# Kernel optimization log

Measured on AMD Instinct MI355X. Metric: run time of the kernel, lower is better.

## Reference

```python
import jax, jax.numpy as jnp
import numpy as np

D = 1024        # embedding_dim
N = 200000      # number of train embeddings
C = 50          # n_concepts
B = 4096        # batch size
NUM_CLASSES = 4
TOPK = 50


def setup_inputs() -> dict:
    key = jax.random.key(0)
    k1, k2, k3, k4, k5 = jax.random.split(key, 5)
    return {
        "concept": jax.random.normal(k1, (D, C), dtype=jnp.float32),
        "train_embeddings": jax.random.normal(k2, (D, N), dtype=jnp.float32),
        "train_embedding": jax.random.normal(k3, (B, D), dtype=jnp.float32),
        "hx_weight": jax.random.normal(k4, (NUM_CLASSES, D), dtype=jnp.float32) * 0.02,
        "hx_bias": jax.random.normal(k5, (NUM_CLASSES,), dtype=jnp.float32) * 0.02,
        "topk": TOPK,
    }


def reference(concept, train_embeddings, train_embedding, hx_weight, hx_bias, topk):
    n_concepts = concept.shape[1]
    k = int(topk)

    # projection of inputs onto concept subspace: P = C (C^T C)^{-1} C^T
    gram = concept.T @ concept                      # (C, C)
    proj_matrix = concept @ jnp.linalg.inv(gram) @ concept.T   # (D, D)
    proj = proj_matrix @ train_embedding.T          # (D, B)
    y_pred = proj.T @ hx_weight.T + hx_bias         # (B, num_classes)
    orig_pred = train_embedding @ hx_weight.T + hx_bias

    # batched KNN: squared euclidean distance of every concept to every train embedding
    # (sqrt is monotone, ordering identical to torch.norm-based distances)
    te_sq = jnp.sum(train_embeddings * train_embeddings, axis=0)   # (N,)
    c_sq = jnp.sum(concept * concept, axis=0)                      # (C,)
    dots = concept.T @ train_embeddings                            # (C, N)
    dist2 = c_sq[:, None] + te_sq[None, :] - 2.0 * dots            # (C, N)
    _, knn_idx = jax.lax.top_k(-dist2, k)                          # (C, k) smallest distances

    # gather neighbor activations: (D, C, k)
    knn_act = jnp.take(train_embeddings, knn_idx.reshape(-1), axis=1).reshape(
        train_embeddings.shape[0], n_concepts, k)

    # L_sparse_1 = mean_c [ sum_{d,k} concept[d,c]*knn[d,c,k] / k ]
    L_sparse_1 = jnp.einsum("dc,dck->", concept, knn_act) / (k * n_concepts)

    eye = jnp.eye(n_concepts, dtype=concept.dtype)
    mask = 1.0 - eye
    L_sparse_2 = jnp.mean(gram * mask)
    norm_metrics = jnp.mean(gram * eye)
    similarity_penalty = jnp.mean(jnp.abs(gram - eye))

    return (orig_pred, y_pred, L_sparse_1, L_sparse_2, norm_metrics, similarity_penalty)
```

## Files before the change

### kernel.cpp

```cpp
#include <hip/hip_runtime.h>
#include <stdint.h>

#define D 1024
#define N 200000
#define C 50
#define B 4096
#define CLS 4
#define KParts 16
#define CAP 4096
#define BN 512
#define NBLK 391
#define NSLOT (NBLK * 8)

typedef __attribute__((ext_vector_type(8))) short short8;
typedef __attribute__((ext_vector_type(4))) float f32x4;

static const size_t OFF_U     = 0;
static const size_t OFF_TESQ  = (size_t)C * N;
static const size_t OFF_GPART = OFF_TESQ + N;
static const size_t OFF_WPART = OFF_GPART + KParts * 2500;
static const size_t OFF_ABF   = ((OFF_WPART + KParts * 200 + 3) / 4) * 4;
static const size_t OFF_RANGE = OFF_ABF + 32768;
static const size_t OFF_SUMS  = OFF_RANGE + 2 * NSLOT;
static const size_t OFF_CNT   = OFF_SUMS + C;
static const size_t OFF_W8    = ((OFF_CNT + 1 + 3) / 4) * 4;

__device__ __forceinline__ unsigned mapf(float v) {
    unsigned u = __float_as_uint(v);
    return (u & 0x80000000u) ? ~u : (u | 0x80000000u);
}
__device__ __forceinline__ float unmapf(unsigned u) {
    unsigned b = (u & 0x80000000u) ? (u ^ 0x80000000u) : ~u;
    return __uint_as_float(b);
}
__device__ __forceinline__ unsigned keyu(float dot, float tesq) {
    return mapf(fmaf(-2.0f, dot, tesq));
}
__device__ __forceinline__ unsigned short f2bf(float f) {
    unsigned u = __float_as_uint(f);
    u += 0x7FFFu + ((u >> 16) & 1u);
    return (unsigned short)(u >> 16);
}
__device__ __forceinline__ float bf2f(unsigned short h) {
    return __uint_as_float((unsigned)h << 16);
}

__global__ __launch_bounds__(256) void kprep(
    const float* __restrict__ concept, const float* __restrict__ hxw,
    float* __restrict__ ws)
{
    int t = threadIdx.x;

    if (blockIdx.x < KParts) {
        __shared__ __align__(16) float ct[64 * 50];
        __shared__ float hs[4 * 64];
        int bid = blockIdx.x;
        int d0 = bid * 64;

        for (int i = t; i < 64 * 50; i += 256) ct[i] = concept[d0 * 50 + i];
        {
            int j = t >> 6, dd = t & 63;
            hs[t] = hxw[j * D + d0 + dd];
        }
        __syncthreads();

        float* gp = ws + OFF_GPART + (size_t)bid * 2500;
        for (int p = t; p < 2500; p += 256) {
            int i = p / 50, j = p - i * 50;
            float acc = 0.f;
            #pragma unroll 8
            for (int dd = 0; dd < 64; ++dd)
                acc = fmaf(ct[dd * 50 + i], ct[dd * 50 + j], acc);
            gp[p] = acc;
        }
        float* wp = ws + OFF_WPART + (size_t)bid * 200;
        if (t < 200) {
            int j = t / 50, c = t - j * 50;
            float acc = 0.f;
            #pragma unroll 8
            for (int dd = 0; dd < 64; ++dd)
                acc = fmaf(hs[j * 64 + dd], ct[dd * 50 + c], acc);
            wp[t] = acc;
        }
        return;
    }

    unsigned short* ap = (unsigned short*)(ws + OFF_ABF);
    for (int idx = t; idx < 8192; idx += 256) {
        int ks = idx >> 8;
        int g  = (idx >> 6) & 3;
        int m  = idx & 63;
        unsigned short v[8];
        #pragma unroll
        for (int j = 0; j < 8; ++j) {
            int k = ks * 32 + g * 8 + j;
            v[j] = (m < 50) ? f2bf(concept[k * 50 + m]) : (unsigned short)0;
        }
        uint4 pk;
        pk.x = (unsigned)v[0] | ((unsigned)v[1] << 16);
        pk.y = (unsigned)v[2] | ((unsigned)v[3] << 16);
        pk.z = (unsigned)v[4] | ((unsigned)v[5] << 16);
        pk.w = (unsigned)v[6] | ((unsigned)v[7] << 16);
        *(uint4*)(ap + (size_t)idx * 8) = pk;
    }
}

__global__ __launch_bounds__(512) void kgemm(
    const float* __restrict__ concept, const float* __restrict__ te,
    const float* __restrict__ hxw, float* __restrict__ ws,
    float* __restrict__ out)
{
    __shared__ unsigned Bl[16 * 516];
    __shared__ __align__(16) unsigned short Al[4 * 64 * 8];
    __shared__ float tsp[4][BN];
    __shared__ float tsf[BN];
    __shared__ float gsh[2500];
    __shared__ float Asv[50 * 56];
    __shared__ float colp[C];
    __shared__ float part[3][8];

    int t = threadIdx.x;
    int l = t & 63, w = t >> 6;

    if (blockIdx.x == NBLK) {
        if (t == 0) ((unsigned*)(ws + OFF_CNT))[0] = 0u;

        float s_all = 0.f, s_tr = 0.f, s_abs = 0.f;
        for (int p = t; p < 2500; p += 512) {
            float g = 0.f;
            #pragma unroll
            for (int b = 0; b < KParts; ++b)
                g += ws[OFF_GPART + (size_t)b * 2500 + p];
            gsh[p] = g;
            int i = p / 50, jj = p - i * 50;
            float e = (i == jj) ? 1.0f : 0.0f;
            s_all += g;
            if (i == jj) s_tr += g;
            s_abs += fabsf(g - e);
        }
        #pragma unroll
        for (int off = 32; off > 0; off >>= 1) {
            s_all += __shfl_down(s_all, off, 64);
            s_tr  += __shfl_down(s_tr,  off, 64);
            s_abs += __shfl_down(s_abs, off, 64);
        }
        if (l == 0) { part[0][w] = s_all; part[1][w] = s_tr; part[2][w] = s_abs; }
        __syncthreads();
        if (t == 0) {
            float a = 0.f, tr = 0.f, ab = 0.f;
            for (int i = 0; i < 8; ++i) { a += part[0][i]; tr += part[1][i]; ab += part[2][i]; }
            out[32769] = (a - tr) / 2500.0f;
            out[32770] = tr / 2500.0f;
            out[32771] = ab / 2500.0f;
        }

        for (int p = t; p < 50 * 56; p += 512) {
            int r = p / 56, col = p - r * 56;
            float v = 0.f;
            if (col < 50) v = gsh[r * 50 + col];
            else if (col < 54) {
                float ww = 0.f;
                #pragma unroll
                for (int b = 0; b < KParts; ++b)
                    ww += ws[OFF_WPART + (size_t)b * 200 + (col - 50) * 50 + r];
                v = ww;
            }
            Asv[p] = v;
        }
        __syncthreads();

        for (int pc = 0; pc < C; ++pc) {
            if (t < C) colp[t] = Asv[t * 56 + pc];
            __syncthreads();
            float pinv = 1.0f / colp[pc];
            if (t < 56) Asv[pc * 56 + t] *= pinv;
            __syncthreads();
            for (int p = t; p < 50 * 56; p += 512) {
                int r = p / 56, col = p - r * 56;
                if (r != pc) Asv[p] = fmaf(-colp[r], Asv[pc * 56 + col], Asv[p]);
            }
            __syncthreads();
        }

        for (int d = t; d < D; d += 512) {
            float wy0 = 0.f, wy1 = 0.f, wy2 = 0.f, wy3 = 0.f;
            for (int c = 0; c < C; ++c) {
                float cv = concept[d * 50 + c];
                wy0 = fmaf(cv, Asv[c * 56 + 50], wy0);
                wy1 = fmaf(cv, Asv[c * 56 + 51], wy1);
                wy2 = fmaf(cv, Asv[c * 56 + 52], wy2);
                wy3 = fmaf(cv, Asv[c * 56 + 53], wy3);
            }
            float4 lo, hi;
            lo.x = hxw[0 * D + d]; lo.y = hxw[1 * D + d];
            lo.z = hxw[2 * D + d]; lo.w = hxw[3 * D + d];
            hi.x = wy0; hi.y = wy1; hi.z = wy2; hi.w = wy3;
            *(float4*)(ws + OFF_W8 + (size_t)d * 8)     = lo;
            *(float4*)(ws + OFF_W8 + (size_t)d * 8 + 4) = hi;
        }
        return;
    }

    int nbase = blockIdx.x * BN;
    int nq = t & 127, rp = t >> 7;
    int ncol0 = nbase + nq * 4;
    bool colv = (ncol0 < N);

    f32x4 accf[4][4];
    #pragma unroll
    for (int mf = 0; mf < 4; ++mf)
        #pragma unroll
        for (int nf = 0; nf < 4; ++nf)
            accf[mf][nf] = (f32x4)(0.0f);
    float ts0 = 0.f, ts1 = 0.f, ts2 = 0.f, ts3 = 0.f;

    const unsigned short* ap = (const unsigned short*)(ws + OFF_ABF);
    int g = l >> 4;

    #pragma unroll 1
    for (int ks = 0; ks < 32; ++ks) {
        __syncthreads();
        if (t < 256) {
            uint4 av = *(const uint4*)(ap + ((size_t)ks * 256 + t) * 8);
            *(uint4*)(Al + t * 8) = av;
        }
        #pragma unroll
        for (int pi = 0; pi < 4; ++pi) {
            int pair = rp + pi * 4;
            int k0 = ks * 32 + pair * 2;
            float4 xa, xb;
            if (colv) {
                xa = *(const float4*)(te + (size_t)k0 * N + ncol0);
                xb = *(const float4*)(te + (size_t)(k0 + 1) * N + ncol0);
            } else {
                xa = make_float4(0.f, 0.f, 0.f, 0.f);
                xb = make_float4(0.f, 0.f, 0.f, 0.f);
            }
            unsigned short a0 = f2bf(xa.x), a1 = f2bf(xa.y), a2 = f2bf(xa.z), a3 = f2bf(xa.w);
            unsigned short b0 = f2bf(xb.x), b1 = f2bf(xb.y), b2 = f2bf(xb.z), b3 = f2bf(xb.w);
            float fa0 = bf2f(a0), fa1 = bf2f(a1), fa2 = bf2f(a2), fa3 = bf2f(a3);
            float fb0 = bf2f(b0), fb1 = bf2f(b1), fb2 = bf2f(b2), fb3 = bf2f(b3);
            ts0 = fmaf(fa0, fa0, fmaf(fb0, fb0, ts0));
            ts1 = fmaf(fa1, fa1, fmaf(fb1, fb1, ts1));
            ts2 = fmaf(fa2, fa2, fmaf(fb2, fb2, ts2));
            ts3 = fmaf(fa3, fa3, fmaf(fb3, fb3, ts3));
            uint4 pk;
            pk.x = (unsigned)a0 | ((unsigned)b0 << 16);
            pk.y = (unsigned)a1 | ((unsigned)b1 << 16);
            pk.z = (unsigned)a2 | ((unsigned)b2 << 16);
            pk.w = (unsigned)a3 | ((unsigned)b3 << 16);
            *(uint4*)(&Bl[pair * 516 + nq * 4]) = pk;
        }
        __syncthreads();

        short8 af[4];
        #pragma unroll
        for (int mf = 0; mf < 4; ++mf)
            af[mf] = *(const short8*)(Al + ((size_t)(g * 64 + mf * 16 + (l & 15))) * 8);
        #pragma unroll
        for (int nf = 0; nf < 4; ++nf) {
            int nn = w * 64 + nf * 16 + (l & 15);
            union { unsigned u[4]; short8 s; } bu;
            bu.u[0] = Bl[(g * 4 + 0) * 516 + nn];
            bu.u[1] = Bl[(g * 4 + 1) * 516 + nn];
            bu.u[2] = Bl[(g * 4 + 2) * 516 + nn];
            bu.u[3] = Bl[(g * 4 + 3) * 516 + nn];
            short8 bv = bu.s;
            #pragma unroll
            for (int mf = 0; mf < 4; ++mf)
                accf[mf][nf] = __builtin_amdgcn_mfma_f32_16x16x32_bf16(
                    af[mf], bv, accf[mf][nf], 0, 0, 0);
        }
    }

    __syncthreads();
    tsp[rp][nq * 4 + 0] = ts0;
    tsp[rp][nq * 4 + 1] = ts1;
    tsp[rp][nq * 4 + 2] = ts2;
    tsp[rp][nq * 4 + 3] = ts3;
    __syncthreads();
    if (t < 128) {
        float4 s;
        s.x = tsp[0][t * 4 + 0] + tsp[1][t * 4 + 0] + tsp[2][t * 4 + 0] + tsp[3][t * 4 + 0];
        s.y = tsp[0][t * 4 + 1] + tsp[1][t * 4 + 1] + tsp[2][t * 4 + 1] + tsp[3][t * 4 + 1];
        s.z = tsp[0][t * 4 + 2] + tsp[1][t * 4 + 2] + tsp[2][t * 4 + 2] + tsp[3][t * 4 + 2];
        s.w = tsp[0][t * 4 + 3] + tsp[1][t * 4 + 3] + tsp[2][t * 4 + 3] + tsp[3][t * 4 + 3];
        *(float4*)(&tsf[t * 4]) = s;
        if (nbase + t * 4 < N)
            *(float4*)(ws + OFF_TESQ + nbase + t * 4) = s;
    }
    __syncthreads();

    unsigned* uws = (unsigned*)ws;
    unsigned kmin = 0xFFFFFFFFu, kmax = 0u;
    #pragma unroll
    for (int mf = 0; mf < 4; ++mf) {
        #pragma unroll
        for (int nf = 0; nf < 4; ++nf) {
            int nloc = w * 64 + nf * 16 + (l & 15);
            int nabs = nbase + nloc;
            #pragma unroll
            for (int r = 0; r < 4; ++r) {
                int c = mf * 16 + (l >> 4) * 4 + r;
                if (c < 50 && nabs < N) {
                    unsigned u = keyu(accf[mf][nf][r], tsf[nloc]);
                    uws[(size_t)c * N + nabs] = u;
                    kmin = min(kmin, u);
                    kmax = max(kmax, u);
                }
            }
        }
    }
    #pragma unroll
    for (int off = 32; off > 0; off >>= 1) {
        kmin = min(kmin, (unsigned)__shfl_down((int)kmin, off, 64));
        kmax = max(kmax, (unsigned)__shfl_down((int)kmax, off, 64));
    }
    if (l == 0) {
        int slot = blockIdx.x * 8 + w;
        ((unsigned*)(ws + OFF_RANGE))[2 * slot]     = kmin;
        ((unsigned*)(ws + OFF_RANGE))[2 * slot + 1] = kmax;
    }
}

__global__ __launch_bounds__(256) void kpred(
    const float* __restrict__ X, const float* __restrict__ hxb,
    const float* __restrict__ ws, float* __restrict__ out)
{
    int t = threadIdx.x;
    int lane = t & 63, w = t >> 6;
    int r = blockIdx.x * 4 + w;
    const float* xr = X + (size_t)r * D;
    const float* w8 = ws + OFF_W8;

    float acc[8];
    #pragma unroll
    for (int j = 0; j < 8; ++j) acc[j] = 0.f;
    #pragma unroll
    for (int i = 0; i < 16; ++i) {
        int d = i * 64 + lane;
        float x = xr[d];
        float4 lo = *(const float4*)(w8 + (size_t)d * 8);
        float4 hi = *(const float4*)(w8 + (size_t)d * 8 + 4);
        acc[0] = fmaf(x, lo.x, acc[0]);
        acc[1] = fmaf(x, lo.y, acc[1]);
        acc[2] = fmaf(x, lo.z, acc[2]);
        acc[3] = fmaf(x, lo.w, acc[3]);
        acc[4] = fmaf(x, hi.x, acc[4]);
        acc[5] = fmaf(x, hi.y, acc[5]);
        acc[6] = fmaf(x, hi.z, acc[6]);
        acc[7] = fmaf(x, hi.w, acc[7]);
    }
    #pragma unroll
    for (int j = 0; j < 8; ++j) {
        float v = acc[j];
        #pragma unroll
        for (int off = 32; off > 0; off >>= 1) v += __shfl_down(v, off, 64);
        if (lane == 0) {
            float b = hxb[j & 3];
            if (j < 4) out[(size_t)r * CLS + j] = v + b;
            else       out[16384 + (size_t)r * CLS + (j - 4)] = v + b;
        }
    }
}

__global__ __launch_bounds__(1024) void k4_select(
    const float* __restrict__ ws, float* __restrict__ wsw,
    float* __restrict__ out, const int* __restrict__ topk)
{
    int c = blockIdx.x, t = threadIdx.x;
    int lane = t & 63, wid = t >> 6;
    const unsigned* uarr = (const unsigned*)ws + (size_t)c * N;
    const float* tesq = ws + OFF_TESQ;

    __shared__ unsigned hist[4096];
    __shared__ unsigned wsum[16], woff[16];
    __shared__ unsigned wmn[16], wmx[16];
    __shared__ unsigned sh_ulo, sh_uhi;
    __shared__ unsigned sh_bin; __shared__ int sh_rem;
    __shared__ int cnt;
    __shared__ unsigned cand_u[CAP];
    __shared__ int      cand_i[CAP];
    __shared__ float fred[16];

    {
        const unsigned* rg = (const unsigned*)(ws + OFF_RANGE);
        unsigned mn = 0xFFFFFFFFu, mx = 0u;
        for (int i = t; i < NSLOT; i += 1024) {
            mn = min(mn, rg[2 * i]);
            mx = max(mx, rg[2 * i + 1]);
        }
        #pragma unroll
        for (int off = 32; off > 0; off >>= 1) {
            mn = min(mn, (unsigned)__shfl_down((int)mn, off, 64));
            mx = max(mx, (unsigned)__shfl_down((int)mx, off, 64));
        }
        if (lane == 0) { wmn[wid] = mn; wmx[wid] = mx; }
        __syncthreads();
        if (t == 0) {
            unsigned m0 = 0xFFFFFFFFu, m1 = 0u;
            for (int w = 0; w < 16; ++w) { m0 = min(m0, wmn[w]); m1 = max(m1, wmx[w]); }
            sh_ulo = m0; sh_uhi = m1;
        }
        __syncthreads();
    }
    unsigned ubase = sh_ulo;
    unsigned ulo = sh_ulo, uhi = sh_uhi;
    int rem = *topk;
    unsigned long long width = (unsigned long long)(uhi - ulo) + 1ull;

    for (int i = t; i < 4096; i += 1024) hist[i] = 0u;
    __syncthreads();
    for (int n = t; n < N; n += 1024) {
        unsigned u = uarr[n];
        unsigned bin = (unsigned)(((unsigned long long)(u - ubase) * 4096ull) / width);
        atomicAdd(&hist[bin], 1u);
    }
    __syncthreads();
    {
        unsigned b0 = (unsigned)t * 4u;
        unsigned h0 = hist[b0], h1 = hist[b0 + 1], h2 = hist[b0 + 2], h3 = hist[b0 + 3];
        unsigned s4 = h0 + h1 + h2 + h3;
        unsigned x = s4;
        #pragma unroll
        for (int off = 1; off < 64; off <<= 1) {
            unsigned y = (unsigned)__shfl_up((int)x, off, 64);
            if (lane >= off) x += y;
        }
        if (lane == 63) wsum[wid] = x;
        __syncthreads();
        if (t == 0) {
            unsigned run = 0;
            for (int w = 0; w < 16; ++w) { woff[w] = run; run += wsum[w]; }
        }
        __syncthreads();
        unsigned cumBefore = woff[wid] + x - s4;
        unsigned remu = (unsigned)rem;
        if (cumBefore < remu && remu <= cumBefore + s4) {
            unsigned cum = cumBefore, bin = b0, r2 = 1;
            unsigned hh[4] = {h0, h1, h2, h3};
            #pragma unroll
            for (int j = 0; j < 4; ++j) {
                if (cum + hh[j] >= remu) { bin = b0 + j; r2 = remu - cum; break; }
                cum += hh[j];
            }
            sh_bin = bin; sh_rem = (int)r2;
        }
        __syncthreads();
        unsigned b = sh_bin;
        rem = sh_rem;
        ulo = ubase + (unsigned)(((unsigned long long)b * width + 4095ull) / 4096ull);
        uhi = ubase + (unsigned)((((unsigned long long)(b + 1) * width + 4095ull) / 4096ull) - 1ull);
        __syncthreads();
    }

    if (t == 0) cnt = 0;
    __syncthreads();
    float lsum = 0.f;
    for (int n = t; n < N; n += 1024) {
        unsigned u = uarr[n];
        if (u < ulo) {
            lsum += 0.5f * (tesq[n] - unmapf(u));
        } else if (u <= uhi) {
            int s = atomicAdd(&cnt, 1);
            if (s < CAP) { cand_u[s] = u; cand_i[s] = n; }
        }
    }
    __syncthreads();
    int cc = cnt < CAP ? cnt : CAP;
    for (int ci = t; ci < cc; ci += 1024) {
        unsigned ui = cand_u[ci]; int ii = cand_i[ci];
        int rank = 0;
        for (int j = 0; j < cc; ++j) {
            unsigned uj = cand_u[j];
            rank += (uj < ui || (uj == ui && cand_i[j] < ii)) ? 1 : 0;
        }
        if (rank < rem) lsum += 0.5f * (tesq[ii] - unmapf(ui));
    }
    #pragma unroll
    for (int off = 32; off > 0; off >>= 1) lsum += __shfl_down(lsum, off, 64);
    if (lane == 0) fred[wid] = lsum;
    __syncthreads();
    if (t == 0) {
        float tot = 0.f;
        for (int w = 0; w < 16; ++w) tot += fred[w];
        wsw[OFF_SUMS + c] = tot;
        __threadfence();
        unsigned done = atomicAdd((unsigned*)(wsw + OFF_CNT), 1u);
        if (done == C - 1) {
            float s = 0.f;
            for (int i = 0; i < C; ++i) s += atomicAdd(&wsw[OFF_SUMS + i], 0.0f);
            out[32768] = s / (float)((*topk) * C);
        }
    }
}

extern "C" void kernel_launch(void* const* d_in, const int* in_sizes, int n_in,
                              void* d_out, int out_size, void* d_ws, size_t ws_size,
                              hipStream_t stream) {
    (void)in_sizes; (void)n_in; (void)out_size; (void)ws_size;
    const float* concept = (const float*)d_in[0];
    const float* te      = (const float*)d_in[1];
    const float* X       = (const float*)d_in[2];
    const float* hxw     = (const float*)d_in[3];
    const float* hxb     = (const float*)d_in[4];
    const int*   topk    = (const int*)d_in[5];
    float* out = (float*)d_out;
    float* ws  = (float*)d_ws;

    kprep<<<dim3(KParts + 1), dim3(256), 0, stream>>>(concept, hxw, ws);
    kgemm<<<dim3(NBLK + 1), dim3(512), 0, stream>>>(concept, te, hxw, ws, out);
    kpred<<<dim3(B / 4), dim3(256), 0, stream>>>(X, hxb, ws, out);
    k4_select<<<dim3(C), dim3(1024), 0, stream>>>(ws, ws, out, topk);
}
```

Baseline: 556.7 us.

## Halve GEMM tile width, double-buffer B tile with register prefetch

Each block now covers 256 columns instead of 512, which doubles the grid. The B tile in LDS is double-buffered: the global loads for the next k-step are issued before the MFMAs and converted afterwards, so one barrier per iteration remains. A fragments are read straight from global instead of being staged in LDS, and shared memory is unioned and reduced so that launch_bounds(512,4) can lift occupancy. The aim is to hide global load latency on the memory-bound scan of the 800MB embeddings. In exchange, per-block overhead rises and the A fragment loads are repeated across blocks.

```diff
diff --git a/kernel.cpp b/kernel.cpp
--- a/kernel.cpp
+++ b/kernel.cpp
@@ -8,9 +8,10 @@
 #define CLS 4
 #define KParts 16
 #define CAP 4096
-#define BN 512
-#define NBLK 391
+#define BN 256
+#define NBLK 782
 #define NSLOT (NBLK * 8)
+#define BLROW 260
 
 typedef __attribute__((ext_vector_type(8))) short short8;
 typedef __attribute__((ext_vector_type(4))) float f32x4;
@@ -105,24 +106,22 @@
     }
 }
 
-__global__ __launch_bounds__(512) void kgemm(
+__global__ __launch_bounds__(512, 4) void kgemm(
     const float* __restrict__ concept, const float* __restrict__ te,
     const float* __restrict__ hxw, float* __restrict__ ws,
     float* __restrict__ out)
 {
-    __shared__ unsigned Bl[16 * 516];
-    __shared__ __align__(16) unsigned short Al[4 * 64 * 8];
-    __shared__ float tsp[4][BN];
-    __shared__ float tsf[BN];
-    __shared__ float gsh[2500];
-    __shared__ float Asv[50 * 56];
-    __shared__ float colp[C];
-    __shared__ float part[3][8];
+    __shared__ __align__(16) unsigned char smem[42496];
 
     int t = threadIdx.x;
     int l = t & 63, w = t >> 6;
 
     if (blockIdx.x == NBLK) {
+        float* gsh  = (float*)smem;
+        float* Asv  = (float*)(smem + 10000);
+        float* colp = (float*)(smem + 21200);
+        float* part = (float*)(smem + 21408);
+
         if (t == 0) ((unsigned*)(ws + OFF_CNT))[0] = 0u;
 
         float s_all = 0.f, s_tr = 0.f, s_abs = 0.f;
@@ -144,11 +143,13 @@
             s_tr  += __shfl_down(s_tr,  off, 64);
             s_abs += __shfl_down(s_abs, off, 64);
         }
-        if (l == 0) { part[0][w] = s_all; part[1][w] = s_tr; part[2][w] = s_abs; }
+        if (l == 0) { part[0 * 8 + w] = s_all; part[1 * 8 + w] = s_tr; part[2 * 8 + w] = s_abs; }
         __syncthreads();
         if (t == 0) {
             float a = 0.f, tr = 0.f, ab = 0.f;
-            for (int i = 0; i < 8; ++i) { a += part[0][i]; tr += part[1][i]; ab += part[2][i]; }
+            for (int i = 0; i < 8; ++i) {
+                a += part[0 * 8 + i]; tr += part[1 * 8 + i]; ab += part[2 * 8 + i];
+            }
             out[32769] = (a - tr) / 2500.0f;
             out[32770] = tr / 2500.0f;
             out[32771] = ab / 2500.0f;
@@ -201,14 +202,18 @@
         return;
     }
 
+    unsigned* Blb = (unsigned*)smem;
+    float* tsp = (float*)(smem + 33280);
+    float* tsf = (float*)(smem + 33280 + 8192);
+
     int nbase = blockIdx.x * BN;
-    int nq = t & 127, rp = t >> 7;
+    int nq = t & 63, rp = w;
     int ncol0 = nbase + nq * 4;
     bool colv = (ncol0 < N);
 
-    f32x4 accf[4][4];
-    #pragma unroll
-    for (int mf = 0; mf < 4; ++mf)
+    f32x4 accf[2][4];
+    #pragma unroll
+    for (int mf = 0; mf < 2; ++mf)
         #pragma unroll
         for (int nf = 0; nf < 4; ++nf)
             accf[mf][nf] = (f32x4)(0.0f);
@@ -216,26 +221,14 @@
 
     const unsigned short* ap = (const unsigned short*)(ws + OFF_ABF);
     int g = l >> 4;
-
-    #pragma unroll 1
-    for (int ks = 0; ks < 32; ++ks) {
-        __syncthreads();
-        if (t < 256) {
-            uint4 av = *(const uint4*)(ap + ((size_t)ks * 256 + t) * 8);
-            *(uint4*)(Al + t * 8) = av;
-        }
-        #pragma unroll
-        for (int pi = 0; pi < 4; ++pi) {
-            int pair = rp + pi * 4;
-            int k0 = ks * 32 + pair * 2;
-            float4 xa, xb;
-            if (colv) {
-                xa = *(const float4*)(te + (size_t)k0 * N + ncol0);
-                xb = *(const float4*)(te + (size_t)(k0 + 1) * N + ncol0);
-            } else {
-                xa = make_float4(0.f, 0.f, 0.f, 0.f);
-                xb = make_float4(0.f, 0.f, 0.f, 0.f);
-            }
+    int mhalf = w >> 2;
+    int nnb = (w & 3) * 64 + (l & 15);
+
+    auto cvt_write = [&](int buf, float4* xr) {
+        #pragma unroll
+        for (int pi = 0; pi < 2; ++pi) {
+            int pair = rp + pi * 8;
+            float4 xa = xr[2 * pi], xb = xr[2 * pi + 1];
             unsigned short a0 = f2bf(xa.x), a1 = f2bf(xa.y), a2 = f2bf(xa.z), a3 = f2bf(xa.w);
             unsigned short b0 = f2bf(xb.x), b1 = f2bf(xb.y), b2 = f2bf(xb.z), b3 = f2bf(xb.w);
             float fa0 = bf2f(a0), fa1 = bf2f(a1), fa2 = bf2f(a2), fa3 = bf2f(a3);
@@ -249,42 +242,68 @@
             pk.y = (unsigned)a1 | ((unsigned)b1 << 16);
             pk.z = (unsigned)a2 | ((unsigned)b2 << 16);
             pk.w = (unsigned)a3 | ((unsigned)b3 << 16);
-            *(uint4*)(&Bl[pair * 516 + nq * 4]) = pk;
-        }
-        __syncthreads();
-
-        short8 af[4];
-        #pragma unroll
-        for (int mf = 0; mf < 4; ++mf)
-            af[mf] = *(const short8*)(Al + ((size_t)(g * 64 + mf * 16 + (l & 15))) * 8);
+            *(uint4*)(&Blb[buf * (16 * BLROW) + pair * BLROW + nq * 4]) = pk;
+        }
+    };
+    auto ldtile = [&](int ks, float4* xr) {
+        #pragma unroll
+        for (int pi = 0; pi < 2; ++pi) {
+            int pair = rp + pi * 8;
+            int k0 = ks * 32 + pair * 2;
+            if (colv) {
+                xr[2 * pi]     = *(const float4*)(te + (size_t)k0 * N + ncol0);
+                xr[2 * pi + 1] = *(const float4*)(te + (size_t)(k0 + 1) * N + ncol0);
+            } else {
+                xr[2 * pi]     = make_float4(0.f, 0.f, 0.f, 0.f);
+                xr[2 * pi + 1] = make_float4(0.f, 0.f, 0.f, 0.f);
+            }
+        }
+    };
+
+    {
+        float4 xr[4];
+        ldtile(0, xr);
+        cvt_write(0, xr);
+    }
+
+    #pragma unroll 1
+    for (int ks = 0; ks < 32; ++ks) {
+        __syncthreads();
+        float4 nx[4];
+        if (ks < 31) ldtile(ks + 1, nx);
+
+        short8 af0 = *(const short8*)(ap + ((size_t)(ks * 4 + g) * 64 + mhalf * 32 + 0 * 16 + (l & 15)) * 8);
+        short8 af1 = *(const short8*)(ap + ((size_t)(ks * 4 + g) * 64 + mhalf * 32 + 1 * 16 + (l & 15)) * 8);
+
+        const unsigned* Bc = Blb + (ks & 1) * (16 * BLROW);
         #pragma unroll
         for (int nf = 0; nf < 4; ++nf) {
-            int nn = w * 64 + nf * 16 + (l & 15);
+            int nn = nnb + nf * 16;
             union { unsigned u[4]; short8 s; } bu;
-            bu.u[0] = Bl[(g * 4 + 0) * 516 + nn];
-            bu.u[1] = Bl[(g * 4 + 1) * 516 + nn];
-            bu.u[2] = Bl[(g * 4 + 2) * 516 + nn];
-            bu.u[3] = Bl[(g * 4 + 3) * 516 + nn];
-            short8 bv = bu.s;
-            #pragma unroll
-            for (int mf = 0; mf < 4; ++mf)
-                accf[mf][nf] = __builtin_amdgcn_mfma_f32_16x16x32_bf16(
-                    af[mf], bv, accf[mf][nf], 0, 0, 0);
-        }
-    }
-
-    __syncthreads();
-    tsp[rp][nq * 4 + 0] = ts0;
-    tsp[rp][nq * 4 + 1] = ts1;
-    tsp[rp][nq * 4 + 2] = ts2;
-    tsp[rp][nq * 4 + 3] = ts3;
-    __syncthreads();
-    if (t < 128) {
-        float4 s;
-        s.x = tsp[0][t * 4 + 0] + tsp[1][t * 4 + 0] + tsp[2][t * 4 + 0] + tsp[3][t * 4 + 0];
-        s.y = tsp[0][t * 4 + 1] + tsp[1][t * 4 + 1] + tsp[2][t * 4 + 1] + tsp[3][t * 4 + 1];
-        s.z = tsp[0][t * 4 + 2] + tsp[1][t * 4 + 2] + tsp[2][t * 4 + 2] + tsp[3][t * 4 + 2];
-        s.w = tsp[0][t * 4 + 3] + tsp[1][t * 4 + 3] + tsp[2][t * 4 + 3] + tsp[3][t * 4 + 3];
+            bu.u[0] = Bc[(g * 4 + 0) * BLROW + nn];
+            bu.u[1] = Bc[(g * 4 + 1) * BLROW + nn];
+            bu.u[2] = Bc[(g * 4 + 2) * BLROW + nn];
+            bu.u[3] = Bc[(g * 4 + 3) * BLROW + nn];
+            accf[0][nf] = __builtin_amdgcn_mfma_f32_16x16x32_bf16(af0, bu.s, accf[0][nf], 0, 0, 0);
+            accf[1][nf] = __builtin_amdgcn_mfma_f32_16x16x32_bf16(af1, bu.s, accf[1][nf], 0, 0, 0);
+        }
+
+        if (ks < 31) cvt_write((ks + 1) & 1, nx);
+    }
+
+    __syncthreads();
+    tsp[rp * 256 + nq * 4 + 0] = ts0;
+    tsp[rp * 256 + nq * 4 + 1] = ts1;
+    tsp[rp * 256 + nq * 4 + 2] = ts2;
+    tsp[rp * 256 + nq * 4 + 3] = ts3;
+    __syncthreads();
+    if (t < 64) {
+        float4 s = make_float4(0.f, 0.f, 0.f, 0.f);
+        #pragma unroll
+        for (int r = 0; r < 8; ++r) {
+            float4 v = *(const float4*)(&tsp[r * 256 + t * 4]);
+            s.x += v.x; s.y += v.y; s.z += v.z; s.w += v.w;
+        }
         *(float4*)(&tsf[t * 4]) = s;
         if (nbase + t * 4 < N)
             *(float4*)(ws + OFF_TESQ + nbase + t * 4) = s;
@@ -294,14 +313,14 @@
     unsigned* uws = (unsigned*)ws;
     unsigned kmin = 0xFFFFFFFFu, kmax = 0u;
     #pragma unroll
-    for (int mf = 0; mf < 4; ++mf) {
+    for (int mf = 0; mf < 2; ++mf) {
         #pragma unroll
         for (int nf = 0; nf < 4; ++nf) {
-            int nloc = w * 64 + nf * 16 + (l & 15);
+            int nloc = nnb + nf * 16;
             int nabs = nbase + nloc;
             #pragma unroll
             for (int r = 0; r < 4; ++r) {
-                int c = mf * 16 + (l >> 4) * 4 + r;
+                int c = mhalf * 32 + mf * 16 + (l >> 4) * 4 + r;
                 if (c < 50 && nabs < N) {
                     unsigned u = keyu(accf[mf][nf][r], tsf[nloc]);
                     uws[(size_t)c * N + nabs] = u;
```

Result: faster. 509.0 us (-8.6%).
